# Kernel optimization log

Measured on AMD Instinct MI355X. Metric: run time of the kernel, lower is better.

Reference implementation:

```python
import jax, jax.numpy as jnp
import numpy as np
import math

D_K = 64

def setup_inputs() -> dict:
    key = jax.random.key(0)
    k1, k2, k3, k4 = jax.random.split(key, 4)
    d = 1024
    x = jax.random.normal(k1, (4, 2048, d), dtype=jnp.float32)
    s = 1.0 / math.sqrt(d)
    Wq = jax.random.normal(k2, (d, D_K), dtype=jnp.float32) * s
    Wk = jax.random.normal(k3, (d, D_K), dtype=jnp.float32) * s
    Wv = jax.random.normal(k4, (d, D_K), dtype=jnp.float32) * s
    return {"x": x, "Wq": Wq, "Wk": Wk, "Wv": Wv}

def reference(x, Wq, Wk, Wv):
    # Q,K,V: [b, s, d_k]
    Q = jnp.einsum('bsd,dk->bsk', x, Wq)
    K = jnp.einsum('bsd,dk->bsk', x, Wk)
    V = jnp.einsum('bsd,dk->bsk', x, Wv)
    scale = 1.0 / math.sqrt(D_K)
    scores = jnp.einsum('bqk,bpk->bqp', Q, K) * scale  # [b, s, s]
    attn = jax.nn.softmax(scores, axis=-1)
    context = jnp.einsum('bqp,bpk->bqk', attn, V)      # [b, s, d_k]
    return context
```

## Files before the change

kernel.cpp:

```cpp
#include <hip/hip_runtime.h>
#include <hip/hip_bf16.h>


typedef __attribute__((ext_vector_type(8))) short bf16x8;
typedef __attribute__((ext_vector_type(4))) float f32x4;
typedef __attribute__((ext_vector_type(4))) unsigned short u16x4;

#define QSCALE 0.1803368801111832f

__device__ __forceinline__ short f2bf(float f) {
    union { float f; unsigned u; } v; v.f = f;
    unsigned r = v.u + 0x7FFF + ((v.u >> 16) & 1);
    return (short)(r >> 16);
}

__device__ __forceinline__ unsigned pk2(float a, float b) {
    union { __hip_bfloat162 h; unsigned u; } v;
    v.h = __float22bfloat162_rn(make_float2(a, b));
    return v.u;
}

__device__ __forceinline__ void gload16(const void* src, void* dst) {
    __builtin_amdgcn_global_load_lds(
        (const __attribute__((address_space(1))) unsigned int*)src,
        (__attribute__((address_space(3))) unsigned int*)dst, 16, 0, 0);
}

__global__ __launch_bounds__(256) void wtrans(const float* __restrict__ Wq,
                                              const float* __restrict__ Wk,
                                              const float* __restrict__ Wv,
                                              short* __restrict__ Wt) {
    __shared__ short lds[64][66];
    int warr = blockIdx.x / 16;
    int d0 = (blockIdx.x % 16) * 64;
    const float* W = (warr == 0) ? Wq : (warr == 1) ? Wk : Wv;
    int rg = threadIdx.x >> 6;
    int c  = threadIdx.x & 63;
    #pragma unroll
    for (int p = 0; p < 16; ++p) {
        int d = p * 4 + rg;
        lds[d][c] = f2bf(W[(d0 + d) * 64 + c]);
    }
    __syncthreads();
    #pragma unroll
    for (int p = 0; p < 16; ++p) {
        int n = p * 4 + rg;
        Wt[(warr * 64 + n) * 1024 + d0 + c] = lds[c][n];
    }
}

__global__ __launch_bounds__(256) void qkv_proj(const float* __restrict__ x,
                                                const short* __restrict__ Wt,
                                                short* __restrict__ Q,
                                                short* __restrict__ K,
                                                short* __restrict__ Vt) {
    __shared__ char stage_lds[3][20480];
    __shared__ short Vlds[32][72];

    int tid = threadIdx.x;
    int wid = tid >> 6, lane = tid & 63;
    int l15 = lane & 15, lg = lane >> 4;
    int wr = wid >> 1, wn = wid & 1;
    int logical = (blockIdx.x & 7) * 64 + (blockIdx.x >> 3);
    int mbase = (logical >> 1) * 32;
    int nbase = (logical & 1) * 96;

    int a_soff[2];
    #pragma unroll
    for (int j = 0; j < 2; ++j) {
        int chunk = wid + j * 4;
        int row = chunk * 4 + (lane >> 4);
        int slot16 = lane & 15;
        int s32 = slot16 >> 1, h16 = slot16 & 1;
        int s32s = s32 ^ (row & 7);
        a_soff[j] = (mbase + row) * 1024 + s32s * 8 + h16 * 4;
    }
    int b_soff[3];
    #pragma unroll
    for (int j = 0; j < 3; ++j) {
        int cb = wid + j * 4;
        int row = cb * 8 + (lane >> 3);
        int slot = lane & 7;
        int ss = slot ^ (row & 7);
        b_soff[j] = (nbase + row) * 1024 + ss * 8;
    }

    f32x4 acc[3];
    #pragma unroll
    for (int f = 0; f < 3; ++f) acc[f] = (f32x4){0.f, 0.f, 0.f, 0.f};

    char* B0 = &stage_lds[0][0];
    char* B1 = &stage_lds[1][0];
    char* B2 = &stage_lds[2][0];

#define STAGE(step, base)                                                    \
    {                                                                        \
        int k0_ = (step) * 64;                                               \
        _Pragma("unroll")                                                    \
        for (int j = 0; j < 2; ++j)                                          \
            gload16(x + a_soff[j] + k0_, (base) + (wid + j * 4) * 1024);     \
        _Pragma("unroll")                                                    \
        for (int j = 0; j < 3; ++j)                                          \
            gload16(Wt + b_soff[j] + k0_, (base) + 8192 + (wid + j * 4) * 1024); \
    }

    STAGE(0, B0);
    STAGE(1, B1);
    asm volatile("s_waitcnt vmcnt(5)" ::: "memory");
    __builtin_amdgcn_s_barrier();
    __builtin_amdgcn_sched_barrier(0);

    for (int t = 0; t < 16; ++t) {
        int cm = t % 3;
        char* cbuf = (cm == 0) ? B0 : (cm == 1) ? B1 : B2;
        if (t + 2 < 16) {
            int nm = (t + 2) % 3;
            char* nbuf = (nm == 0) ? B0 : (nm == 1) ? B1 : B2;
            STAGE(t + 2, nbuf);
        }
        const char* Ab = cbuf;
        const char* Bb = cbuf + 8192;
        int arow = wr * 16 + l15;
        __builtin_amdgcn_s_setprio(1);
        #pragma unroll
        for (int h = 0; h < 2; ++h) {
            int s32s = (h * 4 + lg) ^ (arow & 7);
            const float4* ap = (const float4*)(Ab + arow * 256 + s32s * 32);
            float4 f0 = ap[0];
            float4 f1 = ap[1];
            union { bf16x8 v; unsigned u[4]; } au;
            au.u[0] = pk2(f0.x, f0.y);
            au.u[1] = pk2(f0.z, f0.w);
            au.u[2] = pk2(f1.x, f1.y);
            au.u[3] = pk2(f1.z, f1.w);
            #pragma unroll
            for (int f = 0; f < 3; ++f) {
                int brow = (wn * 3 + f) * 16 + l15;
                int ss = (h * 4 + lg) ^ (brow & 7);
                bf16x8 b = *(const bf16x8*)(Bb + brow * 128 + ss * 16);
                acc[f] = __builtin_amdgcn_mfma_f32_16x16x32_bf16(au.v, b, acc[f], 0, 0, 0);
            }
        }
        __builtin_amdgcn_s_setprio(0);
        if (t < 15) {
            if (t == 14) {
                asm volatile("s_waitcnt vmcnt(0)" ::: "memory");
            } else {
                asm volatile("s_waitcnt vmcnt(5)" ::: "memory");
            }
            __builtin_amdgcn_s_barrier();
            __builtin_amdgcn_sched_barrier(0);
        }
    }
#undef STAGE

    #pragma unroll
    for (int f = 0; f < 3; ++f) {
        int n = nbase + (wn * 3 + f) * 16 + l15;
        #pragma unroll
        for (int r = 0; r < 4; ++r) {
            int ml = wr * 16 + lg * 4 + r;
            int m = mbase + ml;
            float v = acc[f][r];
            if (n < 64) {
                Q[m * 64 + n] = f2bf(v * QSCALE);
            } else if (n < 128) {
                K[m * 64 + (n - 64)] = f2bf(v);
            } else {
                Vlds[ml][n - 128] = f2bf(v);
            }
        }
    }
    if (nbase == 96) {
        __syncthreads();
        int dk = tid >> 2;
        int m0 = (tid & 3) * 8;
        int b_ = mbase >> 11;
        int s_ = mbase & 2047;
        #pragma unroll
        for (int j = 0; j < 2; ++j) {
            u16x4 v;
            #pragma unroll
            for (int i = 0; i < 4; ++i) v[i] = (unsigned short)Vlds[m0 + j * 4 + i][dk];
            *(u16x4*)&Vt[(b_ * 64 + dk) * 2048 + s_ + m0 + j * 4] = v;
        }
    }
}

__global__ __launch_bounds__(512) void attn32(const short* __restrict__ Q,
                                              const short* __restrict__ K,
                                              const short* __restrict__ Vt,
                                              float* __restrict__ out) {
    __shared__ char ubuf[8][8704];
    __shared__ float Mw[8][32];
    __shared__ float Lw[8][32];
    __shared__ float Ltot[32];

    int tid = threadIdx.x, wid = tid >> 6, lane = tid & 63;
    int l15 = lane & 15, lg = lane >> 4;
    int logical = (blockIdx.x & 7) * 32 + (blockIdx.x >> 3);
    int b_ = logical >> 6;
    int q0 = (logical & 63) * 32;
    const short* Kb = K + b_ * 2048 * 64;
    const short* Vb = Vt + b_ * 64 * 2048;

    bf16x8 bq[2][2];
    #pragma unroll
    for (int qg = 0; qg < 2; ++qg) {
        const short* Qp = Q + (b_ * 2048 + q0 + qg * 16 + l15) * 64 + lg * 8;
        bq[qg][0] = *(const bf16x8*)Qp;
        bq[qg][1] = *(const bf16x8*)(Qp + 32);
    }

    short* P = (short*)&ubuf[wid][0];

    f32x4 acc[2][4];
    #pragma unroll
    for (int qg = 0; qg < 2; ++qg)
        #pragma unroll
        for (int t = 0; t < 4; ++t) acc[qg][t] = (f32x4){0.f, 0.f, 0.f, 0.f};
    float m_run[2] = {-INFINITY, -INFINITY};
    float l_run[2] = {0.f, 0.f};

    int kv0 = wid * 256;
    for (int kv = kv0; kv < kv0 + 256; kv += 64) {
        f32x4 s[2][4];
        __builtin_amdgcn_s_setprio(1);
        #pragma unroll
        for (int kt = 0; kt < 4; ++kt) {
            const short* Kp = Kb + (kv + kt * 16 + l15) * 64 + lg * 8;
            bf16x8 ak0 = *(const bf16x8*)Kp;
            bf16x8 ak1 = *(const bf16x8*)(Kp + 32);
            f32x4 z0 = (f32x4){0.f, 0.f, 0.f, 0.f};
            z0 = __builtin_amdgcn_mfma_f32_16x16x32_bf16(ak0, bq[0][0], z0, 0, 0, 0);
            s[0][kt] = __builtin_amdgcn_mfma_f32_16x16x32_bf16(ak1, bq[0][1], z0, 0, 0, 0);
            f32x4 z1 = (f32x4){0.f, 0.f, 0.f, 0.f};
            z1 = __builtin_amdgcn_mfma_f32_16x16x32_bf16(ak0, bq[1][0], z1, 0, 0, 0);
            s[1][kt] = __builtin_amdgcn_mfma_f32_16x16x32_bf16(ak1, bq[1][1], z1, 0, 0, 0);
        }
        __builtin_amdgcn_s_setprio(0);

        #pragma unroll
        for (int qg = 0; qg < 2; ++qg) {
            float m01 = fmaxf(fmaxf(s[qg][0][0], s[qg][0][1]), fmaxf(s[qg][0][2], s[qg][0][3]));
            float m23 = fmaxf(fmaxf(s[qg][1][0], s[qg][1][1]), fmaxf(s[qg][1][2], s[qg][1][3]));
            float m45 = fmaxf(fmaxf(s[qg][2][0], s[qg][2][1]), fmaxf(s[qg][2][2], s[qg][2][3]));
            float m67 = fmaxf(fmaxf(s[qg][3][0], s[qg][3][1]), fmaxf(s[qg][3][2], s[qg][3][3]));
            float mt = fmaxf(fmaxf(m01, m23), fmaxf(m45, m67));
            mt = fmaxf(mt, __shfl_xor(mt, 16));
            mt = fmaxf(mt, __shfl_xor(mt, 32));
            if (!__all(mt - m_run[qg] <= 8.0f)) {
                float mn = fmaxf(m_run[qg], mt);
                float c = exp2f(m_run[qg] - mn);
                m_run[qg] = mn;
                l_run[qg] *= c;
                #pragma unroll
                for (int t = 0; t < 4; ++t)
                    #pragma unroll
                    for (int r = 0; r < 4; ++r) acc[qg][t][r] *= c;
            }
            float rs = 0.f;
            #pragma unroll
            for (int kt = 0; kt < 4; ++kt)
                #pragma unroll
                for (int r = 0; r < 4; ++r) {
                    float p = exp2f(s[qg][kt][r] - m_run[qg]);
                    s[qg][kt][r] = p;
                    rs += p;
                }
            rs += __shfl_xor(rs, 16);
            rs += __shfl_xor(rs, 32);
            l_run[qg] += rs;
        }

        #pragma unroll
        for (int qg = 0; qg < 2; ++qg)
            #pragma unroll
            for (int kt = 0; kt < 4; ++kt) {
                union { u16x4 v; unsigned u[2]; } h;
                h.u[0] = pk2(s[qg][kt][0], s[qg][kt][1]);
                h.u[1] = pk2(s[qg][kt][2], s[qg][kt][3]);
                *(u16x4*)&P[(qg * 16 + l15) * 72 + kt * 16 + lg * 4] = h.v;
            }

        __builtin_amdgcn_s_setprio(1);
        #pragma unroll
        for (int ps = 0; ps < 2; ++ps) {
            bf16x8 bp0 = *(const bf16x8*)&P[l15 * 72 + ps * 32 + lg * 8];
            bf16x8 bp1 = *(const bf16x8*)&P[(16 + l15) * 72 + ps * 32 + lg * 8];
            #pragma unroll
            for (int t = 0; t < 4; ++t) {
                const short* Vp = Vb + (t * 16 + l15) * 2048 + kv + ps * 32 + lg * 8;
                bf16x8 av = *(const bf16x8*)Vp;
                acc[0][t] = __builtin_amdgcn_mfma_f32_16x16x32_bf16(av, bp0, acc[0][t], 0, 0, 0);
                acc[1][t] = __builtin_amdgcn_mfma_f32_16x16x32_bf16(av, bp1, acc[1][t], 0, 0, 0);
            }
        }
        __builtin_amdgcn_s_setprio(0);
    }

    if (lg == 0) {
        #pragma unroll
        for (int qg = 0; qg < 2; ++qg) {
            Mw[wid][qg * 16 + l15] = m_run[qg];
            Lw[wid][qg * 16 + l15] = l_run[qg];
        }
    }
    __syncthreads();

    float* accw = (float*)&ubuf[wid][0];
    #pragma unroll
    for (int qg = 0; qg < 2; ++qg) {
        int row = qg * 16 + l15;
        float m = Mw[0][row];
        #pragma unroll
        for (int w = 1; w < 8; ++w) m = fmaxf(m, Mw[w][row]);
        float fac = exp2f(m_run[qg] - m);
        #pragma unroll
        for (int t = 0; t < 4; ++t) {
            f32x4 v = acc[qg][t];
            v[0] *= fac; v[1] *= fac; v[2] *= fac; v[3] *= fac;
            *(f32x4*)&accw[row * 68 + t * 16 + lg * 4] = v;
        }
    }

    if (wid == 0 && lg == 0) {
        #pragma unroll
        for (int qg = 0; qg < 2; ++qg) {
            int row = qg * 16 + l15;
            float m = Mw[0][row];
            #pragma unroll
            for (int w = 1; w < 8; ++w) m = fmaxf(m, Mw[w][row]);
            float L = 0.f;
            #pragma unroll
            for (int w = 0; w < 8; ++w)
                L += Lw[w][row] * exp2f(Mw[w][row] - m);
            Ltot[row] = L;
        }
    }
    __syncthreads();

    #pragma unroll
    for (int j = 0; j < 4; ++j) {
        int o = tid + j * 512;
        int row = o >> 6, col = o & 63;
        float ssum = 0.f;
        #pragma unroll
        for (int w = 0; w < 8; ++w)
            ssum += ((const float*)&ubuf[w][0])[row * 68 + col];
        out[(b_ * 2048 + q0 + row) * 64 + col] = ssum / Ltot[row];
    }
}

extern "C" void kernel_launch(void* const* d_in, const int* in_sizes, int n_in,
                              void* d_out, int out_size, void* d_ws, size_t ws_size,
                              hipStream_t stream) {
    const float* x  = (const float*)d_in[0];
    const float* Wq = (const float*)d_in[1];
    const float* Wk = (const float*)d_in[2];
    const float* Wv = (const float*)d_in[3];
    float* out = (float*)d_out;

    char* ws = (char*)d_ws;
    short* Wt = (short*)ws;
    short* Q  = (short*)(ws + 393216);
    short* K  = (short*)(ws + 393216 + 1048576);
    short* Vt = (short*)(ws + 393216 + 2 * 1048576);

    hipLaunchKernelGGL(wtrans,   dim3(48),  dim3(256), 0, stream, Wq, Wk, Wv, Wt);
    hipLaunchKernelGGL(qkv_proj, dim3(512), dim3(256), 0, stream, x, Wt, Q, K, Vt);
    hipLaunchKernelGGL(attn32,   dim3(256), dim3(512), 0, stream, Q, K, Vt, out);
}
```

Baseline: 46.16 us.

## Load x tiles via registers, convert to bf16 before staging in LDS

The qkv projection now loads x fp32 tiles into registers one step ahead, converts them to bf16, and writes the packed bf16 to LDS. Previously the raw fp32 tiles were DMA'd directly into LDS and converted on every fragment read. This halves the A-tile LDS footprint, which lets the kernel declare 3 blocks per CU, and it removes the repeated conversion in the MFMA loop. The Vlds transpose buffer now reuses the staging buffer. The cost is more VGPR pressure and register-path global loads, which replace the async LDS DMA for x.

```diff
diff --git a/kernel.cpp b/kernel.cpp
--- a/kernel.cpp
+++ b/kernel.cpp
@@ -49,13 +49,12 @@
     }
 }
 
-__global__ __launch_bounds__(256) void qkv_proj(const float* __restrict__ x,
-                                                const short* __restrict__ Wt,
-                                                short* __restrict__ Q,
-                                                short* __restrict__ K,
-                                                short* __restrict__ Vt) {
-    __shared__ char stage_lds[3][20480];
-    __shared__ short Vlds[32][72];
+__global__ __launch_bounds__(256, 3) void qkv_proj(const float* __restrict__ x,
+                                                   const short* __restrict__ Wt,
+                                                   short* __restrict__ Q,
+                                                   short* __restrict__ K,
+                                                   short* __restrict__ Vt) {
+    __shared__ char stage_lds[3][16384];
 
     int tid = threadIdx.x;
     int wid = tid >> 6, lane = tid & 63;
@@ -65,23 +64,16 @@
     int mbase = (logical >> 1) * 32;
     int nbase = (logical & 1) * 96;
 
-    int a_soff[2];
-    #pragma unroll
-    for (int j = 0; j < 2; ++j) {
-        int chunk = wid + j * 4;
-        int row = chunk * 4 + (lane >> 4);
-        int slot16 = lane & 15;
-        int s32 = slot16 >> 1, h16 = slot16 & 1;
-        int s32s = s32 ^ (row & 7);
-        a_soff[j] = (mbase + row) * 1024 + s32s * 8 + h16 * 4;
-    }
+    int arow_s = tid >> 3, aslot = tid & 7;
+    const float* a_src = x + (mbase + arow_s) * 1024 + aslot * 8;
+    int a_woff = arow_s * 128 + ((aslot ^ (arow_s & 7)) << 4);
+
     int b_soff[3];
     #pragma unroll
     for (int j = 0; j < 3; ++j) {
         int cb = wid + j * 4;
         int row = cb * 8 + (lane >> 3);
-        int slot = lane & 7;
-        int ss = slot ^ (row & 7);
+        int ss = (lane & 7) ^ (row & 7);
         b_soff[j] = (nbase + row) * 1024 + ss * 8;
     }
 
@@ -89,71 +81,71 @@
     #pragma unroll
     for (int f = 0; f < 3; ++f) acc[f] = (f32x4){0.f, 0.f, 0.f, 0.f};
 
-    char* B0 = &stage_lds[0][0];
-    char* B1 = &stage_lds[1][0];
-    char* B2 = &stage_lds[2][0];
-
-#define STAGE(step, base)                                                    \
-    {                                                                        \
-        int k0_ = (step) * 64;                                               \
-        _Pragma("unroll")                                                    \
-        for (int j = 0; j < 2; ++j)                                          \
-            gload16(x + a_soff[j] + k0_, (base) + (wid + j * 4) * 1024);     \
-        _Pragma("unroll")                                                    \
-        for (int j = 0; j < 3; ++j)                                          \
-            gload16(Wt + b_soff[j] + k0_, (base) + 8192 + (wid + j * 4) * 1024); \
-    }
-
-    STAGE(0, B0);
-    STAGE(1, B1);
-    asm volatile("s_waitcnt vmcnt(5)" ::: "memory");
+    float4 areg[2][2];
+
+#define ISSUE(g)                                                              \
+    {                                                                         \
+        const float* ap_ = a_src + (g) * 64;                                  \
+        areg[(g) & 1][0] = *(const float4*)ap_;                               \
+        areg[(g) & 1][1] = *(const float4*)(ap_ + 4);                         \
+        char* bb_ = &stage_lds[(g) % 3][4096];                                \
+        _Pragma("unroll")                                                     \
+        for (int j = 0; j < 3; ++j)                                           \
+            gload16(Wt + b_soff[j] + (g) * 64, bb_ + (wid + j * 4) * 1024);   \
+    }
+
+#define WRITEA(g)                                                             \
+    {                                                                         \
+        float4 f0_ = areg[(g) & 1][0], f1_ = areg[(g) & 1][1];                \
+        union { bf16x8 v; unsigned u[4]; } au_;                               \
+        au_.u[0] = pk2(f0_.x, f0_.y); au_.u[1] = pk2(f0_.z, f0_.w);           \
+        au_.u[2] = pk2(f1_.x, f1_.y); au_.u[3] = pk2(f1_.z, f1_.w);           \
+        *(bf16x8*)(&stage_lds[(g) % 3][0] + a_woff) = au_.v;                  \
+    }
+
+    ISSUE(0);
+    ISSUE(1);
+    WRITEA(0);
+    asm volatile("s_waitcnt vmcnt(5) lgkmcnt(0)" ::: "memory");
     __builtin_amdgcn_s_barrier();
     __builtin_amdgcn_sched_barrier(0);
 
+    #pragma unroll
     for (int t = 0; t < 16; ++t) {
-        int cm = t % 3;
-        char* cbuf = (cm == 0) ? B0 : (cm == 1) ? B1 : B2;
-        if (t + 2 < 16) {
-            int nm = (t + 2) % 3;
-            char* nbuf = (nm == 0) ? B0 : (nm == 1) ? B1 : B2;
-            STAGE(t + 2, nbuf);
-        }
-        const char* Ab = cbuf;
-        const char* Bb = cbuf + 8192;
+        if (t + 2 < 16) ISSUE(t + 2);
+        if (t + 1 < 16) WRITEA(t + 1);
+        const char* Ab = &stage_lds[t % 3][0];
+        const char* Bb = &stage_lds[t % 3][4096];
         int arow = wr * 16 + l15;
         __builtin_amdgcn_s_setprio(1);
         #pragma unroll
         for (int h = 0; h < 2; ++h) {
-            int s32s = (h * 4 + lg) ^ (arow & 7);
-            const float4* ap = (const float4*)(Ab + arow * 256 + s32s * 32);
-            float4 f0 = ap[0];
-            float4 f1 = ap[1];
-            union { bf16x8 v; unsigned u[4]; } au;
-            au.u[0] = pk2(f0.x, f0.y);
-            au.u[1] = pk2(f0.z, f0.w);
-            au.u[2] = pk2(f1.x, f1.y);
-            au.u[3] = pk2(f1.z, f1.w);
+            int sA = (h * 4 + lg) ^ (arow & 7);
+            bf16x8 a = *(const bf16x8*)(Ab + arow * 128 + sA * 16);
             #pragma unroll
             for (int f = 0; f < 3; ++f) {
                 int brow = (wn * 3 + f) * 16 + l15;
                 int ss = (h * 4 + lg) ^ (brow & 7);
                 bf16x8 b = *(const bf16x8*)(Bb + brow * 128 + ss * 16);
-                acc[f] = __builtin_amdgcn_mfma_f32_16x16x32_bf16(au.v, b, acc[f], 0, 0, 0);
+                acc[f] = __builtin_amdgcn_mfma_f32_16x16x32_bf16(a, b, acc[f], 0, 0, 0);
             }
         }
         __builtin_amdgcn_s_setprio(0);
         if (t < 15) {
-            if (t == 14) {
-                asm volatile("s_waitcnt vmcnt(0)" ::: "memory");
+            if (t + 2 < 16) {
+                asm volatile("s_waitcnt vmcnt(5) lgkmcnt(0)" ::: "memory");
             } else {
-                asm volatile("s_waitcnt vmcnt(5)" ::: "memory");
+                asm volatile("s_waitcnt vmcnt(0) lgkmcnt(0)" ::: "memory");
             }
             __builtin_amdgcn_s_barrier();
             __builtin_amdgcn_sched_barrier(0);
         }
     }
-#undef STAGE
-
+#undef ISSUE
+#undef WRITEA
+
+    __syncthreads();
+    short* Vl = (short*)&stage_lds[0][0];
     #pragma unroll
     for (int f = 0; f < 3; ++f) {
         int n = nbase + (wn * 3 + f) * 16 + l15;
@@ -167,7 +159,7 @@
             } else if (n < 128) {
                 K[m * 64 + (n - 64)] = f2bf(v);
             } else {
-                Vlds[ml][n - 128] = f2bf(v);
+                Vl[ml * 72 + (n - 128)] = f2bf(v);
             }
         }
     }
@@ -181,7 +173,7 @@
         for (int j = 0; j < 2; ++j) {
             u16x4 v;
             #pragma unroll
-            for (int i = 0; i < 4; ++i) v[i] = (unsigned short)Vlds[m0 + j * 4 + i][dk];
+            for (int i = 0; i < 4; ++i) v[i] = (unsigned short)Vl[(m0 + j * 4 + i) * 72 + dk];
             *(u16x4*)&Vt[(b_ * 64 + dk) * 2048 + s_ + m0 + j * 4] = v;
         }
     }
```

Measured after the change: 42.69 us. 7.5% less time.
